# Performance work log

Hardware: AMD Instinct MI355X
Metric: run time of the kernel (lower is better)

## Reference

```python
import jax, jax.numpy as jnp
import numpy as np
from jax import lax

B, CIN, H, W = 16, 64, 128, 128
NUM_CLASSES = 80
K = 100              # cfg.TEST.TOPK
SCORE_THRESH = 0.2   # hardcoded in decode()
NMS_THRESH = 0.5     # cfg.TEST.NMS_THRESH
RATIO = 4.0          # inp_downsample_ratio


def setup_inputs() -> dict:
    key = jax.random.key(0)
    ks = jax.random.split(key, 8)
    def w(k, shape, scale=0.05):
        return jax.random.normal(k, shape, dtype=jnp.float32) * scale
    inp = {"x": jax.random.normal(ks[0], (B, CIN, H, W), dtype=jnp.float32)}
    for i, (name, cout) in enumerate([("cls", NUM_CLASSES), ("reg", 2), ("wh", 2)]):
        inp[f"{name}_w1"] = w(ks[1 + 2 * i], (64, CIN, 3, 3))
        inp[f"{name}_b1"] = jnp.zeros((64,), jnp.float32)
        inp[f"{name}_w2"] = w(ks[2 + 2 * i], (cout, 64, 1, 1))
        # cls 1x1 conv bias filled with -2.19 as in the torch module
        inp[f"{name}_b2"] = jnp.full((cout,), -2.19 if name == "cls" else 0.0, jnp.float32)
    return inp


def _conv(x, w, b):
    y = lax.conv_general_dilated(x, w, (1, 1), 'SAME',
                                 dimension_numbers=('NCHW', 'OIHW', 'NCHW'))
    return y + b[None, :, None, None]


def _branch(x, w1, b1, w2, b2):
    return _conv(jax.nn.relu(_conv(x, w1, b1)), w2, b2)


def _nms_keep(boxes, valid):
    # boxes: [K,4] sorted by score desc (top_k output); valid: [K] bool
    x1, y1, x2, y2 = boxes[:, 0], boxes[:, 1], boxes[:, 2], boxes[:, 3]
    area = (x2 - x1) * (y2 - y1)
    iw = jnp.clip(jnp.minimum(x2[:, None], x2[None, :]) - jnp.maximum(x1[:, None], x1[None, :]), 0.0)
    ih = jnp.clip(jnp.minimum(y2[:, None], y2[None, :]) - jnp.maximum(y1[:, None], y1[None, :]), 0.0)
    inter = iw * ih
    iou = inter / (area[:, None] + area[None, :] - inter + 1e-9)  # [K,K]
    idx = jnp.arange(K)
    def step(keep, i):
        sup = (iou[i] > NMS_THRESH) & (idx > i) & keep[i]
        return keep & ~sup, None
    keep, _ = lax.scan(step, valid, idx)
    return keep


def reference(x, cls_w1, cls_b1, cls_w2, cls_b2,
              reg_w1, reg_b1, reg_w2, reg_b2,
              wh_w1, wh_b1, wh_w2, wh_b2):
    cls = jax.nn.sigmoid(_branch(x, cls_w1, cls_b1, cls_w2, cls_b2))  # [B,C,H,W]
    reg = jax.nn.sigmoid(_branch(x, reg_w1, reg_b1, reg_w2, reg_b2))  # [B,2,H,W]
    wh = jnp.exp(_branch(x, wh_w1, wh_b1, wh_w2, wh_b2))              # [B,2,H,W]

    # 3x3 max-pool peak NMS (torch max_pool2d pads with -inf; SAME matches k=3,s=1,p=1)
    pooled = lax.reduce_window(cls, -jnp.inf, lax.max, (1, 1, 3, 3), (1, 1, 1, 1), 'SAME')
    cls = cls * (pooled == cls).astype(cls.dtype)

    cls_f = cls.transpose(0, 2, 3, 1).reshape(B, H * W, NUM_CLASSES)
    reg_f = reg.transpose(0, 2, 3, 1).reshape(B, H * W, 2)
    wh_f = wh.transpose(0, 2, 3, 1).reshape(B, H * W, 2)

    scores_all = jnp.max(cls_f, axis=-1)              # [B,HW]
    cats_all = jnp.argmax(cls_f, axis=-1)             # [B,HW]
    scores, inds = lax.top_k(scores_all, K)           # [B,K], sorted desc
    valid = scores > SCORE_THRESH                     # fixed-size mask instead of dynamic filter

    cats = jnp.take_along_axis(cats_all, inds, axis=1)
    reg_k = jnp.take_along_axis(reg_f, inds[..., None], axis=1)   # [B,K,2]
    wh_k = jnp.take_along_axis(wh_f, inds[..., None], axis=1)     # [B,K,2]

    gy, gx = jnp.meshgrid(jnp.arange(H), jnp.arange(W), indexing='ij')
    grids = jnp.stack([gx, gy], axis=-1).reshape(-1, 2).astype(jnp.float32)  # [HW,2] (x,y)
    ct = grids[inds] + reg_k                                       # [B,K,2]
    boxes = jnp.concatenate([ct - wh_k / 2.0, ct + wh_k / 2.0], axis=-1) * RATIO  # [B,K,4]

    keep = jax.vmap(_nms_keep)(boxes, valid)          # [B,K] bool
    return boxes, cats, scores, keep
```

## Files before the change

kernel.cpp:

```cpp
#include <hip/hip_runtime.h>
#include <math.h>

#define BN 16
#define HWSZ 16384
#define NC 80
#define KK 100

typedef _Float16 f16;
typedef _Float16 f16x2 __attribute__((ext_vector_type(2)));
typedef _Float16 f16x4 __attribute__((ext_vector_type(4)));
typedef _Float16 f16x8 __attribute__((ext_vector_type(8)));
typedef float    f32x4 __attribute__((ext_vector_type(4)));
typedef unsigned int uint;
typedef unsigned long long u64;

#define WS_CLS   0
#define CLS_SZ   (BN*NC*HWSZ)
#define WS_REG   (WS_CLS + CLS_SZ)
#define REG_SZ   (BN*2*HWSZ)
#define WS_WH    (WS_REG + REG_SZ)
#define WH_SZ    (BN*2*HWSZ)
#define WS_SC    (WS_WH + WH_SZ)
#define SC_SZ    (BN*HWSZ)
#define WS_CAT   (WS_SC + SC_SZ)
#define CAT_SZ   (BN*HWSZ)
#define WS_W1H   (WS_CAT + CAT_SZ)
#define W1F      (110592/2)
#define WS_W1L   (WS_W1H + W1F)
#define WS_W2H   (WS_W1L + W1F)
#define W2F      (7168/2)
#define WS_W2L   (WS_W2H + W2F)
#define NREG     (BN*128*2*2)
#define WS_XTH   (WS_W2L + W2F)
#define XT_F     (NREG*2112/2)
#define WS_XTL   (WS_XTH + XT_F)
#define WS_ZR    (WS_XTL + XT_F)
#define ZR_F     1056
#define WS_SC1   (WS_ZR + ZR_F)
#define WS_CAT1  (WS_SC1 + SC_SZ)
#define WS_SC2   (WS_CAT1 + CAT_SZ)
#define WS_CAT2  (WS_SC2 + SC_SZ)
#define WS_SC3   (WS_CAT2 + CAT_SZ)
#define WS_CAT3  (WS_SC3 + SC_SZ)
#define WS_END4  (WS_CAT3 + CAT_SZ)

#define SCL_X   16.0f
#define SCL_W   256.0f
#define INV_ACC (1.0f/4096.0f)

#define GL2LDS(g, l) __builtin_amdgcn_global_load_lds( \
    (__attribute__((address_space(1))) unsigned int*)(unsigned long long)(const void*)(g), \
    (__attribute__((address_space(3))) unsigned int*)(unsigned int)(unsigned long long)(void*)(l), \
    16, 0, 0)

__global__ void k_prep(const float* __restrict__ cw1, const float* __restrict__ rw1,
                       const float* __restrict__ ww1, const float* __restrict__ cw2,
                       const float* __restrict__ rw2, const float* __restrict__ ww2,
                       f16* __restrict__ w1h, f16* __restrict__ w1l,
                       f16* __restrict__ w2h, f16* __restrict__ w2l,
                       float* __restrict__ zr) {
    int idx = blockIdx.x * 256 + threadIdx.x;
    if (idx < 3*9*64*64) {
        int ci = idx & 63, co = (idx >> 6) & 63;
        int s  = (idx >> 12) % 9, br = idx / 36864;
        const float* src = (br == 0) ? cw1 : (br == 1 ? rw1 : ww1);
        float v = src[(co*64 + ci)*9 + s] * SCL_W;
        f16 h = (f16)v;
        w1h[idx] = h; w1l[idx] = (f16)(v - (float)h);
    }
    int j = idx - 3*9*64*64;
    if (j >= 0 && j < 112*64) {
        int ci = j & 63, row = j >> 6;
        float v = 0.f;
        if (row < 80)                    v = cw2[row*64 + ci];
        else if (row < 82)               v = rw2[(row-80)*64 + ci];
        else if (row >= 96 && row < 98)  v = ww2[(row-96)*64 + ci];
        v *= SCL_W;
        f16 h = (f16)v;
        w2h[j] = h; w2l[j] = (f16)(v - (float)h);
    }
    if (zr && idx < ZR_F) zr[idx] = 0.f;
}

__global__ __launch_bounds__(256) void k_prepx(const float* __restrict__ x,
                                               f16* __restrict__ xth,
                                               f16* __restrict__ xtl) {
    const int reg = blockIdx.x;
    const int chunk = reg & 1, hh = (reg >> 1) & 1;
    const int gy = (reg >> 2) & 127, b = reg >> 9;
    __shared__ f16 th[66*72] __attribute__((aligned(16)));
    __shared__ f16 tl[66*72] __attribute__((aligned(16)));
    const int tid = threadIdx.x;
    const float* xb = x + ((size_t)(b*64 + chunk*32))*HWSZ + gy*128;
    #pragma unroll
    for (int it = 0; it < 9; it++) {
        int idx = it*256 + tid;
        if (idx < 2112) {
            int ci = idx / 66, pxi = idx - ci*66;
            int gp = hh*64 - 1 + pxi;
            float v = 0.f;
            if (gp >= 0 && gp < 128) v = xb[(size_t)ci*HWSZ + gp] * SCL_X;
            f16 hv = (f16)v;
            th[pxi*72 + ci] = hv;
            tl[pxi*72 + ci] = (f16)(v - (float)hv);
        }
    }
    __syncthreads();
    f16* oh = xth + (size_t)reg*2112;
    f16* ol = xtl + (size_t)reg*2112;
    {
        int row = tid >> 2, q = tid & 3;
        int sq = q ^ ((row >> 1) & 3);
        *(f16x8*)(oh + row*32 + sq*8) = *(const f16x8*)(th + row*72 + q*8);
        *(f16x8*)(ol + row*32 + sq*8) = *(const f16x8*)(tl + row*72 + q*8);
        if (tid < 8) {
            int u2 = 256 + tid, row2 = u2 >> 2, q2 = u2 & 3;
            int sq2 = q2 ^ ((row2 >> 1) & 3);
            *(f16x8*)(oh + row2*32 + sq2*8) = *(const f16x8*)(th + row2*72 + q2*8);
            *(f16x8*)(ol + row2*32 + sq2*8) = *(const f16x8*)(tl + row2*72 + q2*8);
        }
    }
}

#define ABUF 8448
__global__ __launch_bounds__(256, 2) void k_conv(
    const f16* __restrict__ xth, const f16* __restrict__ xtl, const f16* __restrict__ zreg,
    const f16* __restrict__ w1h, const f16* __restrict__ w1l,
    const f16* __restrict__ w2h, const f16* __restrict__ w2l,
    const float* __restrict__ b1c, const float* __restrict__ b1r, const float* __restrict__ b1w,
    const float* __restrict__ b2c, const float* __restrict__ b2r, const float* __restrict__ b2w,
    float* __restrict__ cls_o, float* __restrict__ reg_o, float* __restrict__ wh_o)
{
    __shared__ char smem[4*ABUF] __attribute__((aligned(16)));
    f16* Rh = (f16*)smem;
    f16* Rl = (f16*)(smem + 9216);

    const int p  = blockIdx.x + 2*blockIdx.y + 128*blockIdx.z;
    const int lg = (p & 7)*256 + (p >> 3);
    const int b  = lg >> 7;
    const int y0 = ((lg & 127) >> 1) * 2;
    const int h  = lg & 1;

    const int tid = threadIdx.x;
    const int w = tid >> 6, lane = tid & 63;
    const int l15 = lane & 15, quad = lane >> 4;
    const int co = w*16 + l15;

    #define STAGE4(ch) do {                                                   \
        _Pragma("unroll")                                                     \
        for (int gyi = 0; gyi < 4; gyi++) {                                   \
            const int gy_ = y0 - 1 + gyi;                                     \
            const f16* sh_; const f16* sl_;                                   \
            if (gy_ >= 0 && gy_ < 128) {                                      \
                size_t ro_ = (size_t)(((b*128 + gy_)*2 + h)*2 + (ch)) * 2112; \
                sh_ = xth + ro_; sl_ = xtl + ro_;                             \
            } else { sh_ = zreg; sl_ = zreg; }                                \
            char* db_ = smem + gyi*ABUF;                                      \
            GL2LDS(sh_ + tid*8, db_ + tid*16);                                \
            GL2LDS(sl_ + tid*8, db_ + 4224 + tid*16);                         \
            if (tid < 8) {                                                    \
                GL2LDS(sh_ + 2048 + tid*8, db_ + 4096 + tid*16);              \
                GL2LDS(sl_ + 2048 + tid*8, db_ + 4224 + 4096 + tid*16);       \
            }                                                                 \
        }                                                                     \
    } while (0)

    f32x4 accA[3][4], accB[3][4];
    #pragma unroll
    for (int br = 0; br < 3; br++)
        #pragma unroll
        for (int m = 0; m < 4; m++) {
            accA[br][m] = (f32x4){0.f,0.f,0.f,0.f};
            accB[br][m] = (f32x4){0.f,0.f,0.f,0.f};
        }

    #define COMPUTE(ph) do {                                                  \
        for (int r = 0; r < 3; r++) {                                         \
            const f16* A0 = (const f16*)(smem + r*ABUF);                      \
            const f16* A1 = (const f16*)(smem + (r+1)*ABUF);                  \
            _Pragma("unroll")                                                 \
            for (int dx = 0; dx < 3; dx++) {                                  \
                const int s = r*3 + dx;                                       \
                f16x8 bh[3], bl[3];                                           \
                _Pragma("unroll")                                             \
                for (int br = 0; br < 3; br++) {                              \
                    size_t k = ((size_t)((br*9 + s)*64 + co))*64 + (ph)*32 + quad*8; \
                    bh[br] = *(const f16x8*)(w1h + k);                        \
                    bl[br] = *(const f16x8*)(w1l + k);                        \
                }                                                             \
                _Pragma("unroll")                                             \
                for (int m = 0; m < 4; m++) {                                 \
                    const int row = m*16 + l15 + dx;                          \
                    const int off = row*32 + ((quad ^ ((row >> 1) & 3)) << 3);\
                    {                                                         \
                        f16x8 ah0 = *(const f16x8*)(A0 + off);                \
                        f16x8 al0 = *(const f16x8*)(A0 + 2112 + off);         \
                        _Pragma("unroll")                                     \
                        for (int br = 0; br < 3; br++) {                      \
                            accA[br][m] = __builtin_amdgcn_mfma_f32_16x16x32_f16(ah0, bh[br], accA[br][m], 0,0,0); \
                            accA[br][m] = __builtin_amdgcn_mfma_f32_16x16x32_f16(ah0, bl[br], accA[br][m], 0,0,0); \
                            accA[br][m] = __builtin_amdgcn_mfma_f32_16x16x32_f16(al0, bh[br], accA[br][m], 0,0,0); \
                        }                                                     \
                    }                                                         \
                    {                                                         \
                        f16x8 ah1 = *(const f16x8*)(A1 + off);                \
                        f16x8 al1 = *(const f16x8*)(A1 + 2112 + off);         \
                        _Pragma("unroll")                                     \
                        for (int br = 0; br < 3; br++) {                      \
                            accB[br][m] = __builtin_amdgcn_mfma_f32_16x16x32_f16(ah1, bh[br], accB[br][m], 0,0,0); \
                            accB[br][m] = __builtin_amdgcn_mfma_f32_16x16x32_f16(ah1, bl[br], accB[br][m], 0,0,0); \
                            accB[br][m] = __builtin_amdgcn_mfma_f32_16x16x32_f16(al1, bh[br], accB[br][m], 0,0,0); \
                        }                                                     \
                    }                                                         \
                }                                                             \
            }                                                                 \
        }                                                                     \
    } while (0)

    STAGE4(0);
    __syncthreads();
    COMPUTE(0);
    __syncthreads();
    STAGE4(1);
    __syncthreads();
    COMPUTE(1);

    #undef STAGE4
    #undef COMPUTE

    #define EPIROW(ACC, yy) do {                                              \
        __syncthreads();                        \
        _Pragma("unroll")                                                     \
        for (int m = 0; m < 4; m++)                                           \
            _Pragma("unroll")                                                 \
            for (int rg = 0; rg < 4; rg++) {                                  \
                float t = fmaxf(ACC[br][m][rg]*INV_ACC + b1v, 0.f) * SCL_X;   \
                f16 hh = (f16)t;                                              \
                int pxl = m*16 + quad*4 + rg;                                 \
                Rh[pxl*72 + co] = hh;                                         \
                Rl[pxl*72 + co] = (f16)(t - (float)hh);                       \
            }                                                                 \
        __syncthreads();                                                      \
        const int NT     = (br == 0) ? 5 : 1;                                 \
        const int rowoff = (br == 0) ? 0 : (br == 1 ? 80 : 96);               \
        f32x4 a2[5];                                                          \
        _Pragma("unroll")                                                     \
        for (int n = 0; n < 5; n++) a2[n] = (f32x4){0.f,0.f,0.f,0.f};         \
        _Pragma("unroll")                                                     \
        for (int kc = 0; kc < 64; kc += 32) {                                 \
            int off = co*72 + kc + quad*8;                                    \
            f16x8 xh = *(const f16x8*)(Rh + off);                             \
            f16x8 xl = *(const f16x8*)(Rl + off);                             \
            _Pragma("unroll")                                                 \
            for (int n = 0; n < 5; n++) {                                     \
                if (n >= NT) break;                                           \
                const f16* g2h = w2h + (rowoff + n*16 + l15)*64 + kc + quad*8;\
                const f16* g2l = w2l + (rowoff + n*16 + l15)*64 + kc + quad*8;\
                f16x8 bh2 = *(const f16x8*)g2h;                               \
                f16x8 bl2 = *(const f16x8*)g2l;                               \
                a2[n] = __builtin_amdgcn_mfma_f32_16x16x32_f16(xh, bh2, a2[n], 0,0,0); \
                a2[n] = __builtin_amdgcn_mfma_f32_16x16x32_f16(xh, bl2, a2[n], 0,0,0); \
                a2[n] = __builtin_amdgcn_mfma_f32_16x16x32_f16(xl, bh2, a2[n], 0,0,0); \
            }                                                                 \
        }                                                                     \
        const int pxg = h*64 + w*16 + quad*4;                                 \
        if (br == 0) {                                                        \
            _Pragma("unroll")                                                 \
            for (int n = 0; n < 5; n++) {                                     \
                int co2 = n*16 + l15;                                         \
                float bb = b2c[co2];                                          \
                _Pragma("unroll")                                             \
                for (int rg = 0; rg < 4; rg++) {                              \
                    float sv = a2[n][rg]*INV_ACC + bb;                        \
                    cls_o[((size_t)(b*80 + co2)*128 + (yy))*128 + pxg + rg] = 1.f/(1.f + expf(-sv)); \
                }                                                             \
            }                                                                 \
        } else {                                                              \
            if (l15 < 2) {                                                    \
                const float* b2 = (br == 1) ? b2r : b2w;                      \
                float* outp     = (br == 1) ? reg_o : wh_o;                   \
                float bb = b2[l15];                                           \
                _Pragma("unroll")                                             \
                for (int rg = 0; rg < 4; rg++) {                              \
                    float sv = a2[0][rg]*INV_ACC + bb;                        \
                    float o  = (br == 1) ? (1.f/(1.f + expf(-sv))) : expf(sv);\
                    outp[((size_t)(b*2 + l15))*HWSZ + (yy)*128 + pxg + rg] = o; \
                }                                                             \
            }                                                                 \
        }                                                                     \
    } while (0)

    #pragma unroll
    for (int br = 0; br < 3; br++) {
        const float* b1 = (br == 0) ? b1c : (br == 1 ? b1r : b1w);
        const float b1v = b1[co];
        EPIROW(accA, y0);
        EPIROW(accB, y0 + 1);
    }
    #undef EPIROW
}

#define A_STRIDE 36
#define ABUF_FB  9504
__global__ __launch_bounds__(256) void k_conv_fb(
    const float* __restrict__ x,
    const f16* __restrict__ w1h, const f16* __restrict__ w1l,
    const f16* __restrict__ w2h, const f16* __restrict__ w2l,
    const float* __restrict__ b1c, const float* __restrict__ b1r, const float* __restrict__ b1w,
    const float* __restrict__ b2c, const float* __restrict__ b2r, const float* __restrict__ b2w,
    float* __restrict__ cls_o, float* __restrict__ reg_o, float* __restrict__ wh_o)
{
    __shared__ char smem[19008] __attribute__((aligned(16)));
    f16* Rh = (f16*)smem;
    f16* Rl = (f16*)(smem + 9216);

    const int h = blockIdx.x, y = blockIdx.y, b = blockIdx.z;
    const int tid = threadIdx.x;
    const int w = tid >> 6, lane = tid & 63;
    const int l15 = lane & 15, quad = lane >> 4;

    static const int CS[6] = {0,0,0,1,1,1};
    static const int RS[6] = {0,1,2,0,1,2};

    #define STAGEF(bufi, si_) do {                                            \
        const int gy = y - 1 + RS[si_];                                       \
        const bool ok = (gy >= 0) && (gy < 128);                              \
        const float* xp = x + ((size_t)(b*64 + CS[si_]*32)*128 + gy)*128;     \
        f16x2* dh = (f16x2*)(smem + (bufi)*ABUF_FB);                          \
        f16x2* dl = (f16x2*)(smem + (bufi)*ABUF_FB + 4752);                   \
        _Pragma("unroll")                                                     \
        for (int e0 = 0; e0 < 1024; e0 += 256) {                              \
            int e = e0 + tid;                                                 \
            int pxl = e & 63, cp = e >> 6;                                    \
            float v0 = 0.f, v1 = 0.f;                                         \
            if (ok) { int g = h*64 + pxl;                                     \
                      v0 = xp[(size_t)(2*cp)*HWSZ + g]*SCL_X;                 \
                      v1 = xp[(size_t)(2*cp+1)*HWSZ + g]*SCL_X; }             \
            f16 h0 = (f16)v0, h1 = (f16)v1;                                   \
            f16 l0 = (f16)(v0 - (float)h0), l1 = (f16)(v1 - (float)h1);       \
            int wi = (pxl + 1)*18 + cp;                                       \
            dh[wi] = (f16x2){h0, h1};                                         \
            dl[wi] = (f16x2){l0, l1};                                         \
        }                                                                     \
        if (tid < 32) {                                                       \
            int side = tid >> 4, cp = tid & 15;                               \
            bool valid = ok && (side ? (h == 0) : (h == 1));                  \
            int g = side ? 64 : 63;                                           \
            float v0 = 0.f, v1 = 0.f;                                         \
            if (valid) { v0 = xp[(size_t)(2*cp)*HWSZ + g]*SCL_X;              \
                         v1 = xp[(size_t)(2*cp+1)*HWSZ + g]*SCL_X; }          \
            f16 h0 = (f16)v0, h1 = (f16)v1;                                   \
            f16 l0 = (f16)(v0 - (float)h0), l1 = (f16)(v1 - (float)h1);       \
            int wi = (side ? 65 : 0)*18 + cp;                                 \
            dh[wi] = (f16x2){h0, h1};                                         \
            dl[wi] = (f16x2){l0, l1};                                         \
        }                                                                     \
    } while (0)

    f32x4 acc[3][4];
    #pragma unroll
    for (int br = 0; br < 3; br++)
        #pragma unroll
        for (int m = 0; m < 4; m++) acc[br][m] = (f32x4){0.f,0.f,0.f,0.f};

    STAGEF(0, 0);
    __syncthreads();

    for (int si = 0; si < 6; si++) {
        const int cur = si & 1;
        if (si < 5) STAGEF(cur ^ 1, si + 1);
        const f16* APh = (const f16*)(smem + cur*ABUF_FB);
        const f16* APl = APh + 2376;
        const int chunk = CS[si], r = RS[si];
        #pragma unroll
        for (int dx = 0; dx < 3; dx++) {
            const int s = r*3 + dx;
            f16x8 bh[3], bl[3];
            #pragma unroll
            for (int br = 0; br < 3; br++) {
                size_t k = ((size_t)((br*9 + s)*64 + (w*16 + l15)))*64 + chunk*32 + quad*8;
                bh[br] = *(const f16x8*)(w1h + k);
                bl[br] = *(const f16x8*)(w1l + k);
            }
            #pragma unroll
            for (int m = 0; m < 4; m++) {
                int off = (m*16 + l15 + dx)*A_STRIDE + quad*8;
                f16x4 h0 = *(const f16x4*)(APh + off);
                f16x4 h1 = *(const f16x4*)(APh + off + 4);
                f16x4 u0 = *(const f16x4*)(APl + off);
                f16x4 u1 = *(const f16x4*)(APl + off + 4);
                f16x8 ah = __builtin_shufflevector(h0, h1, 0,1,2,3,4,5,6,7);
                f16x8 al = __builtin_shufflevector(u0, u1, 0,1,2,3,4,5,6,7);
                #pragma unroll
                for (int br = 0; br < 3; br++) {
                    acc[br][m] = __builtin_amdgcn_mfma_f32_16x16x32_f16(ah, bh[br], acc[br][m], 0,0,0);
                    acc[br][m] = __builtin_amdgcn_mfma_f32_16x16x32_f16(ah, bl[br], acc[br][m], 0,0,0);
                    acc[br][m] = __builtin_amdgcn_mfma_f32_16x16x32_f16(al, bh[br], acc[br][m], 0,0,0);
                }
            }
        }
        __syncthreads();
    }
    #undef STAGEF

    #pragma unroll
    for (int br = 0; br < 3; br++) {
        const float* b1 = (br == 0) ? b1c : (br == 1 ? b1r : b1w);
        const float b1v = b1[w*16 + l15];
        __syncthreads();
        #pragma unroll
        for (int m = 0; m < 4; m++)
            #pragma unroll
            for (int rg = 0; rg < 4; rg++) {
                float t = fmaxf(acc[br][m][rg]*INV_ACC + b1v, 0.f) * SCL_X;
                f16 hh = (f16)t;
                int pxl = m*16 + quad*4 + rg;
                int co  = w*16 + l15;
                Rh[pxl*72 + co] = hh;
                Rl[pxl*72 + co] = (f16)(t - (float)hh);
            }
        __syncthreads();

        const int NT     = (br == 0) ? 5 : 1;
        const int rowoff = (br == 0) ? 0 : (br == 1 ? 80 : 96);
        f32x4 a2[5];
        #pragma unroll
        for (int n = 0; n < 5; n++) a2[n] = (f32x4){0.f,0.f,0.f,0.f};

        #pragma unroll
        for (int kc = 0; kc < 64; kc += 32) {
            int off = (w*16 + l15)*72 + kc + quad*8;
            f16x8 xh = *(const f16x8*)(Rh + off);
            f16x8 xl = *(const f16x8*)(Rl + off);
            #pragma unroll
            for (int n = 0; n < 5; n++) {
                if (n >= NT) break;
                const f16* g2h = w2h + (rowoff + n*16 + l15)*64 + kc + quad*8;
                const f16* g2l = w2l + (rowoff + n*16 + l15)*64 + kc + quad*8;
                f16x8 bh = *(const f16x8*)g2h;
                f16x8 bl = *(const f16x8*)g2l;
                a2[n] = __builtin_amdgcn_mfma_f32_16x16x32_f16(xh, bh, a2[n], 0,0,0);
                a2[n] = __builtin_amdgcn_mfma_f32_16x16x32_f16(xh, bl, a2[n], 0,0,0);
                a2[n] = __builtin_amdgcn_mfma_f32_16x16x32_f16(xl, bh, a2[n], 0,0,0);
            }
        }

        const int pxg = h*64 + w*16 + quad*4;
        if (br == 0) {
            #pragma unroll
            for (int n = 0; n < 5; n++) {
                int co2 = n*16 + l15;
                float bb = b2c[co2];
                #pragma unroll
                for (int rg = 0; rg < 4; rg++) {
                    float sv = a2[n][rg]*INV_ACC + bb;
                    cls_o[((size_t)(b*80 + co2)*128 + y)*128 + pxg + rg] = 1.f/(1.f + expf(-sv));
                }
            }
        } else {
            if (l15 < 2) {
                const float* b2 = (br == 1) ? b2r : b2w;
                float* outp     = (br == 1) ? reg_o : wh_o;
                float bb = b2[l15];
                #pragma unroll
                for (int rg = 0; rg < 4; rg++) {
                    float sv = a2[0][rg]*INV_ACC + bb;
                    float o  = (br == 1) ? (1.f/(1.f + expf(-sv))) : expf(sv);
                    outp[((size_t)(b*2 + l15))*HWSZ + y*128 + pxg + rg] = o;
                }
            }
        }
    }
}

__global__ __launch_bounds__(256) void k_peaks(const float* __restrict__ cls,
                                               float* __restrict__ scA, int* __restrict__ catA,
                                               float* __restrict__ scB, int* __restrict__ catB,
                                               float* __restrict__ scC, int* __restrict__ catC,
                                               float* __restrict__ scD, int* __restrict__ catD,
                                               int span) {
    const int b  = blockIdx.y;
    const int z  = blockIdx.z;
    const int c0 = z * span, c1 = c0 + span;
    float* __restrict__ sc  = (z == 0) ? scA  : (z == 1) ? scB  : (z == 2) ? scC  : scD;
    int*   __restrict__ cat = (z == 0) ? catA : (z == 1) ? catB : (z == 2) ? catC : catD;
    const int wv = threadIdx.x >> 6;
    const int l  = threadIdx.x & 63;
    const int y0 = blockIdx.x * 16 + wv * 4;
    const int p0 = l * 2;
    const bool gt = (y0 > 0);
    const bool gb = (y0 + 4 < 128);
    float best[8]; int bc[8];
    #pragma unroll
    for (int i = 0; i < 8; i++) { best[i] = -1.f; bc[i] = c0; }
    for (int c = c0; c < c1; c++) {
        const float* pl = cls + (size_t)(b*80 + c)*HWSZ + y0*128 + p0;
        float2 t[6];
        t[0] = gt ? *(const float2*)(pl - 128) : make_float2(-1e30f, -1e30f);
        t[1] = *(const float2*)pl;
        t[2] = *(const float2*)(pl + 128);
        t[3] = *(const float2*)(pl + 256);
        t[4] = *(const float2*)(pl + 384);
        t[5] = gb ? *(const float2*)(pl + 512) : make_float2(-1e30f, -1e30f);
        #pragma unroll
        for (int i = 0; i < 4; i++) {
            float vm0 = fmaxf(t[i+1].x, fmaxf(t[i].x, t[i+2].x));
            float vm1 = fmaxf(t[i+1].y, fmaxf(t[i].y, t[i+2].y));
            float lft = __shfl_up(vm1, 1);   if (l == 0)  lft = -1e30f;
            float rgt = __shfl_down(vm0, 1); if (l == 63) rgt = -1e30f;
            float m0 = fmaxf(lft, fmaxf(vm0, vm1));
            float m1 = fmaxf(vm0, fmaxf(vm1, rgt));
            float k0 = (t[i+1].x == m0) ? t[i+1].x : 0.f;
            float k1 = (t[i+1].y == m1) ? t[i+1].y : 0.f;
            if (k0 > best[2*i])   { best[2*i]   = k0; bc[2*i]   = c; }
            if (k1 > best[2*i+1]) { best[2*i+1] = k1; bc[2*i+1] = c; }
        }
    }
    #pragma unroll
    for (int i = 0; i < 4; i++) {
        int o = b*HWSZ + (y0 + i)*128 + p0;
        *(float2*)&sc[o] = make_float2(best[2*i], best[2*i+1]);
        *(int2*)&cat[o]  = make_int2(bc[2*i], bc[2*i+1]);
    }
}

__global__ __launch_bounds__(256) void k_merge4(float* __restrict__ sc0, int* __restrict__ cat0,
                                                const float* __restrict__ s1, const int* __restrict__ c1,
                                                const float* __restrict__ s2, const int* __restrict__ c2,
                                                const float* __restrict__ s3, const int* __restrict__ c3) {
    int i = (blockIdx.x * 256 + threadIdx.x) * 4;
    float4 a = *(const float4*)(sc0 + i);
    int4   ca = *(const int4*)(cat0 + i);
    {
        float4 bq = *(const float4*)(s1 + i);
        int4   cb = *(const int4*)(c1 + i);
        if (bq.x > a.x) { a.x = bq.x; ca.x = cb.x; }
        if (bq.y > a.y) { a.y = bq.y; ca.y = cb.y; }
        if (bq.z > a.z) { a.z = bq.z; ca.z = cb.z; }
        if (bq.w > a.w) { a.w = bq.w; ca.w = cb.w; }
    }
    {
        float4 bq = *(const float4*)(s2 + i);
        int4   cb = *(const int4*)(c2 + i);
        if (bq.x > a.x) { a.x = bq.x; ca.x = cb.x; }
        if (bq.y > a.y) { a.y = bq.y; ca.y = cb.y; }
        if (bq.z > a.z) { a.z = bq.z; ca.z = cb.z; }
        if (bq.w > a.w) { a.w = bq.w; ca.w = cb.w; }
    }
    {
        float4 bq = *(const float4*)(s3 + i);
        int4   cb = *(const int4*)(c3 + i);
        if (bq.x > a.x) { a.x = bq.x; ca.x = cb.x; }
        if (bq.y > a.y) { a.y = bq.y; ca.y = cb.y; }
        if (bq.z > a.z) { a.z = bq.z; ca.z = cb.z; }
        if (bq.w > a.w) { a.w = bq.w; ca.w = cb.w; }
    }
    *(float4*)(sc0 + i) = a;
    *(int4*)(cat0 + i)  = ca;
}

__global__ __launch_bounds__(256) void k_select(const float* __restrict__ sc,
                                                const int* __restrict__ cats,
                                                const float* __restrict__ regp,
                                                const float* __restrict__ whp,
                                                float* __restrict__ out) {
    const int b   = blockIdx.x;
    const int tid = threadIdx.x;
    const int wv  = tid >> 6, lane = tid & 63;
    const float* scb = sc + (size_t)b*HWSZ;

    __shared__ int   red[2][4];
    __shared__ uint  wtot[4];
    __shared__ int   gib[128];
    __shared__ uint  gvb[128];
    __shared__ int   ebuf[KK];
    __shared__ u64   keys[128];
    __shared__ int   s_inds[KK];
    __shared__ float s_vals[KK];
    __shared__ float X1[KK], Y1[KK], X2[KK], Y2[KK], AR[KK];

    f32x4 d[16];
    #pragma unroll
    for (int c = 0; c < 16; c++)
        d[c] = *(const f32x4*)(scb + c*1024 + tid*4);

    #define CNT_GT(T, OUTV) do {                                              \
        int myc_ = 0;                                                         \
        _Pragma("unroll")                                                     \
        for (int c = 0; c < 16; c++) {                                        \
            _Pragma("unroll")                                                 \
            for (int j = 0; j < 4; j++)                                       \
                myc_ += (__float_as_uint(d[c][j]) > (T)) ? 1 : 0;             \
        }                                                                     \
        _Pragma("unroll")                                                     \
        for (int o_ = 32; o_ >= 1; o_ >>= 1) myc_ += __shfl_xor(myc_, o_);    \
        if (lane == 0) red[par][wv] = myc_;                                   \
        __syncthreads();                                                      \
        OUTV = red[par][0] + red[par][1] + red[par][2] + red[par][3];         \
        par ^= 1;                                                             \
    } while (0)

    int par = 0;
    uint Vbits; uint G;
    {
        int tot0; CNT_GT(0u, tot0);
        if (tot0 < KK) { Vbits = 0u; G = (uint)tot0; }
        else {
            uint lo = 0u, hi = 0x7F800000u; int gHi = 0;
            while (hi - lo > 1u) {
                uint mid = lo + ((hi - lo) >> 1);
                int t_; CNT_GT(mid, t_);
                if (t_ >= KK) lo = mid; else { hi = mid; gHi = t_; }
            }
            Vbits = hi; G = (uint)gHi;
        }
    }
    #undef CNT_GT
    const uint Eneed = KK - G;

    f32x4 c4[16];
    #pragma unroll
    for (int c = 0; c < 16; c++)
        c4[c] = *(const f32x4*)(scb + tid*64 + c*4);

    uint cntG = 0, cntE = 0;
    #pragma unroll
    for (int c = 0; c < 16; c++)
        #pragma unroll
        for (int j = 0; j < 4; j++) {
            uint u = __float_as_uint(c4[c][j]);
            cntG += (u > Vbits) ? 1u : 0u;
            cntE += (u == Vbits) ? 1u : 0u;
        }
    uint pk = (cntE << 16) | cntG;
    uint v = pk;
    #pragma unroll
    for (int o = 1; o <= 32; o <<= 1) {
        uint ov = __shfl_up(v, o);
        if (lane >= o) v += ov;
    }
    if (lane == 63) wtot[wv] = v;
    __syncthreads();
    uint woff = 0;
    for (int i = 0; i < 4; i++) if (i < wv) woff += wtot[i];
    uint excl = v - pk + woff;
    uint pG = excl & 0xFFFFu, pE = excl >> 16;

    #pragma unroll
    for (int c = 0; c < 16; c++)
        #pragma unroll
        for (int j = 0; j < 4; j++) {
            uint u = __float_as_uint(c4[c][j]);
            int idx = tid*64 + c*4 + j;
            if (u > Vbits) { gib[pG] = idx; gvb[pG] = u; pG++; }
            else if (u == Vbits) { if (pE < Eneed) ebuf[pE] = idx; pE++; }
        }
    __syncthreads();

    if (tid < 128)
        keys[tid] = (tid < (int)G) ? (((u64)(~gvb[tid]) << 32) | (uint)gib[tid])
                                   : ~0ull;
    for (uint k2 = 2; k2 <= 128; k2 <<= 1) {
        for (uint j = k2 >> 1; j > 0; j >>= 1) {
            __syncthreads();
            if (tid < 128) {
                uint i = (uint)tid, ixj = i ^ j;
                if (ixj > i) {
                    u64 a = keys[i], bb = keys[ixj];
                    bool up = ((i & k2) == 0);
                    if ((a > bb) == up) { keys[i] = bb; keys[ixj] = a; }
                }
            }
        }
    }
    __syncthreads();

    if (tid < KK) {
        if (tid < (int)G) {
            u64 kk2 = keys[tid];
            s_inds[tid] = (int)(uint)kk2;
            s_vals[tid] = __uint_as_float(~(uint)(kk2 >> 32));
        } else {
            s_inds[tid] = ebuf[tid - (int)G];
            s_vals[tid] = __uint_as_float(Vbits);
        }
    }
    __syncthreads();

    if (tid < KK) {
        int ind   = s_inds[tid];
        float scv = s_vals[tid];
        const float* rb = regp + (size_t)b*2*HWSZ;
        const float* wb = whp  + (size_t)b*2*HWSZ;
        float r0 = rb[ind], r1 = rb[HWSZ + ind];
        float w0 = wb[ind], w1 = wb[HWSZ + ind];
        float ctx = (float)(ind & 127) + r0;
        float cty = (float)(ind >> 7) + r1;
        float x1 = (ctx - w0*0.5f)*4.f, y1 = (cty - w1*0.5f)*4.f;
        float x2 = (ctx + w0*0.5f)*4.f, y2 = (cty + w1*0.5f)*4.f;
        size_t bo = ((size_t)b*KK + tid)*4;
        out[bo+0] = x1; out[bo+1] = y1; out[bo+2] = x2; out[bo+3] = y2;
        out[BN*KK*4 + b*KK + tid]         = (float)cats[(size_t)b*HWSZ + ind];
        out[BN*KK*4 + BN*KK + b*KK + tid] = scv;
        X1[tid] = x1; Y1[tid] = y1; X2[tid] = x2; Y2[tid] = y2;
        AR[tid] = (x2 - x1)*(y2 - y1);
    }
    __syncthreads();

    if (tid < 64) {
        const int l = tid;
        float x1a = X1[l], y1a = Y1[l], x2a = X2[l], y2a = Y2[l], ara = AR[l];
        int   ka  = (s_vals[l] > 0.2f) ? 1 : 0;
        float x1b = 0, y1b = 0, x2b = 0, y2b = 0, arb = 0;
        int   kb  = 0;
        if (l < KK - 64) {
            x1b = X1[64+l]; y1b = Y1[64+l]; x2b = X2[64+l]; y2b = Y2[64+l];
            arb = AR[64+l];
            kb  = (s_vals[64+l] > 0.2f) ? 1 : 0;
        }
        for (int i = 0; i < KK; i++) {
            float jx1, jy1, jx2, jy2, jar; int jk;
            if (i < 64) {
                jx1 = __shfl(x1a, i); jy1 = __shfl(y1a, i);
                jx2 = __shfl(x2a, i); jy2 = __shfl(y2a, i);
                jar = __shfl(ara, i); jk  = __shfl(ka,  i);
            } else {
                int li = i - 64;
                jx1 = __shfl(x1b, li); jy1 = __shfl(y1b, li);
                jx2 = __shfl(x2b, li); jy2 = __shfl(y2b, li);
                jar = __shfl(arb, li); jk  = __shfl(kb,  li);
            }
            if (jk) {
                if (ka && l > i) {
                    float iw = fminf(jx2, x2a) - fmaxf(jx1, x1a); iw = iw > 0.f ? iw : 0.f;
                    float ih = fminf(jy2, y2a) - fmaxf(jy1, y1a); ih = ih > 0.f ? ih : 0.f;
                    float inter = iw*ih;
                    float iou = inter / (jar + ara - inter + 1e-9f);
                    if (iou > 0.5f) ka = 0;
                }
                if (kb && (64 + l) > i) {
                    float iw = fminf(jx2, x2b) - fmaxf(jx1, x1b); iw = iw > 0.f ? iw : 0.f;
                    float ih = fminf(jy2, y2b) - fmaxf(jy1, y1b); ih = ih > 0.f ? ih : 0.f;
                    float inter = iw*ih;
                    float iou = inter / (jar + arb - inter + 1e-9f);
                    if (iou > 0.5f) kb = 0;
                }
            }
        }
        int koff = BN*KK*4 + 2*BN*KK;
        out[koff + b*KK + l] = ka ? 1.f : 0.f;
        if (l < KK - 64) out[koff + b*KK + 64 + l] = kb ? 1.f : 0.f;
    }
}

extern "C" void kernel_launch(void* const* d_in, const int* in_sizes, int n_in,
                              void* d_out, int out_size, void* d_ws, size_t ws_size,
                              hipStream_t stream) {
    const float* x      = (const float*)d_in[0];
    const float* cls_w1 = (const float*)d_in[1];
    const float* cls_b1 = (const float*)d_in[2];
    const float* cls_w2 = (const float*)d_in[3];
    const float* cls_b2 = (const float*)d_in[4];
    const float* reg_w1 = (const float*)d_in[5];
    const float* reg_b1 = (const float*)d_in[6];
    const float* reg_w2 = (const float*)d_in[7];
    const float* reg_b2 = (const float*)d_in[8];
    const float* wh_w1  = (const float*)d_in[9];
    const float* wh_b1  = (const float*)d_in[10];
    const float* wh_w2  = (const float*)d_in[11];
    const float* wh_b2  = (const float*)d_in[12];

    float* ws   = (float*)d_ws;
    float* clsb = ws + WS_CLS;
    float* regb = ws + WS_REG;
    float* whb  = ws + WS_WH;
    float* scw  = ws + WS_SC;
    int*   cat  = (int*)(ws + WS_CAT);
    f16*   w1h  = (f16*)(ws + WS_W1H);
    f16*   w1l  = (f16*)(ws + WS_W1L);
    f16*   w2h  = (f16*)(ws + WS_W2H);
    f16*   w2l  = (f16*)(ws + WS_W2L);
    f16*   xth  = (f16*)(ws + WS_XTH);
    f16*   xtl  = (f16*)(ws + WS_XTL);
    f16*   zr   = (f16*)(ws + WS_ZR);
    float* sc1  = ws + WS_SC1;
    int*   cat1 = (int*)(ws + WS_CAT1);
    float* sc2  = ws + WS_SC2;
    int*   cat2 = (int*)(ws + WS_CAT2);
    float* sc3  = ws + WS_SC3;
    int*   cat3 = (int*)(ws + WS_CAT3);
    float* out  = (float*)d_out;

    const bool big = ws_size >= (size_t)WS_END4 * 4u;

    k_prep<<<(3*9*64*64 + 112*64 + 255)/256, 256, 0, stream>>>(
        cls_w1, reg_w1, wh_w1, cls_w2, reg_w2, wh_w2, w1h, w1l, w2h, w2l,
        big ? (float*)(ws + WS_ZR) : (float*)0);
    if (big) {
        k_prepx<<<NREG, 256, 0, stream>>>(x, xth, xtl);
        k_conv<<<dim3(2, 64, 16), 256, 0, stream>>>(
            xth, xtl, zr, w1h, w1l, w2h, w2l, cls_b1, reg_b1, wh_b1,
            cls_b2, reg_b2, wh_b2, clsb, regb, whb);
        k_peaks<<<dim3(8, 16, 4), 256, 0, stream>>>(
            clsb, scw, cat, sc1, cat1, sc2, cat2, sc3, cat3, 20);
        k_merge4<<<256, 256, 0, stream>>>(scw, cat, sc1, cat1, sc2, cat2, sc3, cat3);
    } else {
        k_conv_fb<<<dim3(2, 128, 16), 256, 0, stream>>>(
            x, w1h, w1l, w2h, w2l, cls_b1, reg_b1, wh_b1,
            cls_b2, reg_b2, wh_b2, clsb, regb, whb);
        k_peaks<<<dim3(8, 16, 1), 256, 0, stream>>>(
            clsb, scw, cat, scw, cat, scw, cat, scw, cat, 80);
    }
    k_select<<<16, 256, 0, stream>>>(scw, cat, regb, whb, out);
}
```

Measured before the change: 441.9 us.

## Prefetch second channel half into extra LDS buffers and enlarge peak tiles

After: 427.4 us. 3.3% less time.

```diff
diff --git a/kernel.cpp b/kernel.cpp
--- a/kernel.cpp
+++ b/kernel.cpp
@@ -131,7 +131,7 @@
     const float* __restrict__ b2c, const float* __restrict__ b2r, const float* __restrict__ b2w,
     float* __restrict__ cls_o, float* __restrict__ reg_o, float* __restrict__ wh_o)
 {
-    __shared__ char smem[4*ABUF] __attribute__((aligned(16)));
+    __shared__ char smem[7*ABUF] __attribute__((aligned(16)));
     f16* Rh = (f16*)smem;
     f16* Rl = (f16*)(smem + 9216);
 
@@ -146,22 +146,19 @@
     const int l15 = lane & 15, quad = lane >> 4;
     const int co = w*16 + l15;
 
-    #define STAGE4(ch) do {                                                   \
-        _Pragma("unroll")                                                     \
-        for (int gyi = 0; gyi < 4; gyi++) {                                   \
-            const int gy_ = y0 - 1 + gyi;                                     \
-            const f16* sh_; const f16* sl_;                                   \
-            if (gy_ >= 0 && gy_ < 128) {                                      \
-                size_t ro_ = (size_t)(((b*128 + gy_)*2 + h)*2 + (ch)) * 2112; \
-                sh_ = xth + ro_; sl_ = xtl + ro_;                             \
-            } else { sh_ = zreg; sl_ = zreg; }                                \
-            char* db_ = smem + gyi*ABUF;                                      \
-            GL2LDS(sh_ + tid*8, db_ + tid*16);                                \
-            GL2LDS(sl_ + tid*8, db_ + 4224 + tid*16);                         \
-            if (tid < 8) {                                                    \
-                GL2LDS(sh_ + 2048 + tid*8, db_ + 4096 + tid*16);              \
-                GL2LDS(sl_ + 2048 + tid*8, db_ + 4224 + 4096 + tid*16);       \
-            }                                                                 \
+    #define STAGE1(ch, gyi, bufi) do {                                        \
+        const int gy_ = y0 - 1 + (gyi);                                       \
+        const f16* sh_; const f16* sl_;                                       \
+        if (gy_ >= 0 && gy_ < 128) {                                          \
+            size_t ro_ = (size_t)(((b*128 + gy_)*2 + h)*2 + (ch)) * 2112;     \
+            sh_ = xth + ro_; sl_ = xtl + ro_;                                 \
+        } else { sh_ = zreg; sl_ = zreg; }                                    \
+        char* db_ = smem + (bufi)*ABUF;                                       \
+        GL2LDS(sh_ + tid*8, db_ + tid*16);                                    \
+        GL2LDS(sl_ + tid*8, db_ + 4224 + tid*16);                             \
+        if (tid < 8) {                                                        \
+            GL2LDS(sh_ + 2048 + tid*8, db_ + 4096 + tid*16);                  \
+            GL2LDS(sl_ + 2048 + tid*8, db_ + 4224 + 4096 + tid*16);           \
         }                                                                     \
     } while (0)
 
@@ -174,59 +171,67 @@
             accB[br][m] = (f32x4){0.f,0.f,0.f,0.f};
         }
 
-    #define COMPUTE(ph) do {                                                  \
-        for (int r = 0; r < 3; r++) {                                         \
-            const f16* A0 = (const f16*)(smem + r*ABUF);                      \
-            const f16* A1 = (const f16*)(smem + (r+1)*ABUF);                  \
+    #define CSTEP(ph, rr, A0p, A1p) do {                                      \
+        const f16* A0 = (const f16*)(A0p);                                    \
+        const f16* A1 = (const f16*)(A1p);                                    \
+        _Pragma("unroll")                                                     \
+        for (int dx = 0; dx < 3; dx++) {                                      \
+            const int s = (rr)*3 + dx;                                        \
+            f16x8 bh[3], bl[3];                                               \
             _Pragma("unroll")                                                 \
-            for (int dx = 0; dx < 3; dx++) {                                  \
-                const int s = r*3 + dx;                                       \
-                f16x8 bh[3], bl[3];                                           \
-                _Pragma("unroll")                                             \
-                for (int br = 0; br < 3; br++) {                              \
-                    size_t k = ((size_t)((br*9 + s)*64 + co))*64 + (ph)*32 + quad*8; \
-                    bh[br] = *(const f16x8*)(w1h + k);                        \
-                    bl[br] = *(const f16x8*)(w1l + k);                        \
+            for (int br = 0; br < 3; br++) {                                  \
+                size_t k = ((size_t)((br*9 + s)*64 + co))*64 + (ph)*32 + quad*8; \
+                bh[br] = *(const f16x8*)(w1h + k);                            \
+                bl[br] = *(const f16x8*)(w1l + k);                            \
+            }                                                                 \
+            _Pragma("unroll")                                                 \
+            for (int m = 0; m < 4; m++) {                                     \
+                const int row = m*16 + l15 + dx;                              \
+                const int off = row*32 + ((quad ^ ((row >> 1) & 3)) << 3);    \
+                {                                                             \
+                    f16x8 ah0 = *(const f16x8*)(A0 + off);                    \
+                    f16x8 al0 = *(const f16x8*)(A0 + 2112 + off);             \
+                    _Pragma("unroll")                                         \
+                    for (int br = 0; br < 3; br++) {                          \
+                        accA[br][m] = __builtin_amdgcn_mfma_f32_16x16x32_f16(ah0, bh[br], accA[br][m], 0,0,0); \
+                        accA[br][m] = __builtin_amdgcn_mfma_f32_16x16x32_f16(ah0, bl[br], accA[br][m], 0,0,0); \
+                        accA[br][m] = __builtin_amdgcn_mfma_f32_16x16x32_f16(al0, bh[br], accA[br][m], 0,0,0); \
+                    }                                                         \
                 }                                                             \
-                _Pragma("unroll")                                             \
-                for (int m = 0; m < 4; m++) {                                 \
-                    const int row = m*16 + l15 + dx;                          \
-                    const int off = row*32 + ((quad ^ ((row >> 1) & 3)) << 3);\
-                    {                                                         \
-                        f16x8 ah0 = *(const f16x8*)(A0 + off);                \
-                        f16x8 al0 = *(const f16x8*)(A0 + 2112 + off);         \
-                        _Pragma("unroll")                                     \
-                        for (int br = 0; br < 3; br++) {                      \
-                            accA[br][m] = __builtin_amdgcn_mfma_f32_16x16x32_f16(ah0, bh[br], accA[br][m], 0,0,0); \
-                            accA[br][m] = __builtin_amdgcn_mfma_f32_16x16x32_f16(ah0, bl[br], accA[br][m], 0,0,0); \
-                            accA[br][m] = __builtin_amdgcn_mfma_f32_16x16x32_f16(al0, bh[br], accA[br][m], 0,0,0); \
-                        }                                                     \
-                    }                                                         \
-                    {                                                         \
-                        f16x8 ah1 = *(const f16x8*)(A1 + off);                \
-                        f16x8 al1 = *(const f16x8*)(A1 + 2112 + off);         \
-                        _Pragma("unroll")                                     \
-                        for (int br = 0; br < 3; br++) {                      \
-                            accB[br][m] = __builtin_amdgcn_mfma_f32_16x16x32_f16(ah1, bh[br], accB[br][m], 0,0,0); \
-                            accB[br][m] = __builtin_amdgcn_mfma_f32_16x16x32_f16(ah1, bl[br], accB[br][m], 0,0,0); \
-                            accB[br][m] = __builtin_amdgcn_mfma_f32_16x16x32_f16(al1, bh[br], accB[br][m], 0,0,0); \
-                        }                                                     \
+                {                                                             \
+                    f16x8 ah1 = *(const f16x8*)(A1 + off);                    \
+                    f16x8 al1 = *(const f16x8*)(A1 + 2112 + off);             \
+                    _Pragma("unroll")                                         \
+                    for (int br = 0; br < 3; br++) {                          \
+                        accB[br][m] = __builtin_amdgcn_mfma_f32_16x16x32_f16(ah1, bh[br], accB[br][m], 0,0,0); \
+                        accB[br][m] = __builtin_amdgcn_mfma_f32_16x16x32_f16(ah1, bl[br], accB[br][m], 0,0,0); \
+                        accB[br][m] = __builtin_amdgcn_mfma_f32_16x16x32_f16(al1, bh[br], accB[br][m], 0,0,0); \
                     }                                                         \
                 }                                                             \
             }                                                                 \
         }                                                                     \
     } while (0)
 
-    STAGE4(0);
-    __syncthreads();
-    COMPUTE(0);
-    __syncthreads();
-    STAGE4(1);
-    __syncthreads();
-    COMPUTE(1);
-
-    #undef STAGE4
-    #undef COMPUTE
+    #pragma unroll
+    for (int gyi = 0; gyi < 4; gyi++) STAGE1(0, gyi, gyi);
+    #pragma unroll
+    for (int gyi = 0; gyi < 3; gyi++) STAGE1(1, gyi, 4 + gyi);
+    __syncthreads();
+
+    for (int r = 0; r < 3; r++)
+        CSTEP(0, r, smem + r*ABUF, smem + (r+1)*ABUF);
+
+    __syncthreads();
+    STAGE1(1, 3, 0);
+
+    for (int r = 0; r < 2; r++)
+        CSTEP(1, r, smem + (4+r)*ABUF, smem + (5+r)*ABUF);
+
+    __syncthreads();
+    CSTEP(1, 2, smem + 6*ABUF, smem + 0*ABUF);
+
+    #undef STAGE1
+    #undef CSTEP
 
     #define EPIROW(ACC, yy) do {                                              \
         __syncthreads();                        \
@@ -486,24 +491,22 @@
     int*   __restrict__ cat = (z == 0) ? catA : (z == 1) ? catB : (z == 2) ? catC : catD;
     const int wv = threadIdx.x >> 6;
     const int l  = threadIdx.x & 63;
-    const int y0 = blockIdx.x * 16 + wv * 4;
+    const int y0 = blockIdx.x * 32 + wv * 8;
     const int p0 = l * 2;
     const bool gt = (y0 > 0);
-    const bool gb = (y0 + 4 < 128);
-    float best[8]; int bc[8];
-    #pragma unroll
-    for (int i = 0; i < 8; i++) { best[i] = -1.f; bc[i] = c0; }
+    const bool gb = (y0 + 8 < 128);
+    float best[16]; int bc[16];
+    #pragma unroll
+    for (int i = 0; i < 16; i++) { best[i] = -1.f; bc[i] = c0; }
     for (int c = c0; c < c1; c++) {
         const float* pl = cls + (size_t)(b*80 + c)*HWSZ + y0*128 + p0;
-        float2 t[6];
+        float2 t[10];
         t[0] = gt ? *(const float2*)(pl - 128) : make_float2(-1e30f, -1e30f);
-        t[1] = *(const float2*)pl;
-        t[2] = *(const float2*)(pl + 128);
-        t[3] = *(const float2*)(pl + 256);
-        t[4] = *(const float2*)(pl + 384);
-        t[5] = gb ? *(const float2*)(pl + 512) : make_float2(-1e30f, -1e30f);
-        #pragma unroll
-        for (int i = 0; i < 4; i++) {
+        #pragma unroll
+        for (int i = 0; i < 8; i++) t[i+1] = *(const float2*)(pl + i*128);
+        t[9] = gb ? *(const float2*)(pl + 8*128) : make_float2(-1e30f, -1e30f);
+        #pragma unroll
+        for (int i = 0; i < 8; i++) {
             float vm0 = fmaxf(t[i+1].x, fmaxf(t[i].x, t[i+2].x));
             float vm1 = fmaxf(t[i+1].y, fmaxf(t[i].y, t[i+2].y));
             float lft = __shfl_up(vm1, 1);   if (l == 0)  lft = -1e30f;
@@ -517,7 +520,7 @@
         }
     }
     #pragma unroll
-    for (int i = 0; i < 4; i++) {
+    for (int i = 0; i < 8; i++) {
         int o = b*HWSZ + (y0 + i)*128 + p0;
         *(float2*)&sc[o] = make_float2(best[2*i], best[2*i+1]);
         *(int2*)&cat[o]  = make_int2(bc[2*i], bc[2*i+1]);
@@ -801,14 +804,14 @@
         k_conv<<<dim3(2, 64, 16), 256, 0, stream>>>(
             xth, xtl, zr, w1h, w1l, w2h, w2l, cls_b1, reg_b1, wh_b1,
             cls_b2, reg_b2, wh_b2, clsb, regb, whb);
-        k_peaks<<<dim3(8, 16, 4), 256, 0, stream>>>(
+        k_peaks<<<dim3(4, 16, 4), 256, 0, stream>>>(
             clsb, scw, cat, sc1, cat1, sc2, cat2, sc3, cat3, 20);
         k_merge4<<<256, 256, 0, stream>>>(scw, cat, sc1, cat1, sc2, cat2, sc3, cat3);
     } else {
         k_conv_fb<<<dim3(2, 128, 16), 256, 0, stream>>>(
             x, w1h, w1l, w2h, w2l, cls_b1, reg_b1, wh_b1,
             cls_b2, reg_b2, wh_b2, clsb, regb, whb);
-        k_peaks<<<dim3(8, 16, 1), 256, 0, stream>>>(
+        k_peaks<<<dim3(4, 16, 1), 256, 0, stream>>>(
             clsb, scw, cat, scw, cat, scw, cat, scw, cat, 80);
     }
     k_select<<<16, 256, 0, stream>>>(scw, cat, regb, whb, out);
```
